# Kernel tuning notes

Measured on AMD Instinct MI355X. Metric: run time of the kernel, lower is better.

## Reference

```python
import jax, jax.numpy as jnp
import numpy as np

DIM = 1024
NUM_HEADS = 16
HEAD_DIM = DIM // NUM_HEADS
SCALING = HEAD_DIM ** (-0.5)


def setup_inputs() -> dict:
    key = jax.random.key(0)
    ks = jax.random.split(key, 9)
    B, S = 2, 2048
    s = DIM ** -0.5  # ~ torch Linear init scale
    inp = {
        "x": jax.random.normal(ks[0], (B, S, DIM), dtype=jnp.float32),
        "wq": jax.random.uniform(ks[1], (DIM, DIM), jnp.float32, -s, s),
        "bq": jax.random.uniform(ks[2], (DIM,), jnp.float32, -s, s),
        "wk": jax.random.uniform(ks[3], (DIM, DIM), jnp.float32, -s, s),
        "bk": jax.random.uniform(ks[4], (DIM,), jnp.float32, -s, s),
        "wv": jax.random.uniform(ks[5], (DIM, DIM), jnp.float32, -s, s),
        "bv": jax.random.uniform(ks[6], (DIM,), jnp.float32, -s, s),
        "wo": jax.random.uniform(ks[7], (DIM, DIM), jnp.float32, -s, s),
        "bo": jax.random.uniform(ks[8], (DIM,), jnp.float32, -s, s),
    }
    return inp


def reference(x, wq, bq, wk, bk, wv, bv, wo, bo):
    B, S, D = x.shape
    # projections (weights stored [out,in] like torch Linear -> x @ W.T + b)
    q = (x @ wq.T + bq).reshape(B, S, NUM_HEADS, HEAD_DIM)
    k = (x @ wk.T + bk).reshape(B, S, NUM_HEADS, HEAD_DIM)
    v = (x @ wv.T + bv).reshape(B, S, NUM_HEADS, HEAD_DIM)
    # [B,H,S,S] scores, scaled
    scores = jnp.einsum("bqhd,bkhd->bhqk", q, k) * SCALING
    attn = jax.nn.softmax(scores, axis=-1)
    # dropout p=0.0 (eval): identity
    out = jnp.einsum("bhqk,bkhd->bqhd", attn, v).reshape(B, S, D)
    return out @ wo.T + bo
```

## Files before the change

kernel.cpp:

```cpp
#include <hip/hip_runtime.h>

#define DIM 1024
#define NHEADS 16
#define HDIM 64
#define BATCH 2
#define SEQ 2048
#define MTOT (BATCH*SEQ)
#define QSCALE 0.18033688011112042f
#define XN ((size_t)MTOT*DIM)
#define WN ((size_t)DIM*DIM)

typedef __attribute__((ext_vector_type(8))) short short8;
typedef __attribute__((ext_vector_type(4))) float f32x4;
typedef __attribute__((ext_vector_type(16))) float f32x16;
typedef __attribute__((ext_vector_type(2))) int int2v;

static __device__ __forceinline__ unsigned short bf16rne(float f) {
    unsigned u = __builtin_bit_cast(unsigned, f);
    return (unsigned short)((u + 0x7fffu + ((u >> 16) & 1u)) >> 16);
}

static __device__ __forceinline__ void gld16(const void* g, void* l) {
    __builtin_amdgcn_global_load_lds((const __attribute__((address_space(1))) void*)g,
                                     (__attribute__((address_space(3))) void*)l, 16, 0, 0);
}

static __device__ __forceinline__ f32x16 mfma32(short8 a, short8 b, f32x16 c) {
    return __builtin_amdgcn_mfma_f32_32x32x16_bf16(a, b, c, 0, 0, 0);
}

__global__ __launch_bounds__(256)
void prep(const float* __restrict__ x, const float* __restrict__ wq, const float* __restrict__ wk,
          const float* __restrict__ wv, const float* __restrict__ wo, unsigned short* __restrict__ dst)
{
    const size_t i = ((size_t)blockIdx.x*256 + threadIdx.x)*8;
    const float* s; size_t o;
    if (i < XN)           { s = x;  o = i; }
    else if (i < XN+WN)   { s = wq; o = i - XN; }
    else if (i < XN+2*WN) { s = wk; o = i - XN - WN; }
    else if (i < XN+3*WN) { s = wv; o = i - XN - 2*WN; }
    else                  { s = wo; o = i - XN - 3*WN; }
    float4 a = *(const float4*)(s + o);
    float4 b = *(const float4*)(s + o + 4);
    uint4 w;
    w.x = (unsigned)bf16rne(a.x) | ((unsigned)bf16rne(a.y) << 16);
    w.y = (unsigned)bf16rne(a.z) | ((unsigned)bf16rne(a.w) << 16);
    w.z = (unsigned)bf16rne(b.x) | ((unsigned)bf16rne(b.y) << 16);
    w.w = (unsigned)bf16rne(b.z) | ((unsigned)bf16rne(b.w) << 16);
    *(uint4*)&dst[i] = w;
}

__global__ __launch_bounds__(256)
void gemm_qkv(const unsigned short* __restrict__ A,
              const unsigned short* __restrict__ W0, const unsigned short* __restrict__ W1,
              const unsigned short* __restrict__ W2,
              const float* __restrict__ b0, const float* __restrict__ b1, const float* __restrict__ b2,
              unsigned short* __restrict__ o0, unsigned short* __restrict__ o1, unsigned short* __restrict__ o2)
{
    __shared__ __align__(16) unsigned short As[4][4096];
    __shared__ __align__(16) unsigned short Bs[4][4096];
    const int t = threadIdx.x, wid = t >> 6, lane = t & 63;
    const int lr = lane & 15, lg = lane >> 4;
    const int bid = blockIdx.y * 24 + blockIdx.x;
    const int swz = (bid & 7) * 96 + (bid >> 3);
    const int sx = swz % 24, sy = swz / 24;
    const int widx = sx >> 3;
    const int n0 = (sx & 7) << 7;
    const int m0 = sy << 7;
    const unsigned short* W = widx == 0 ? W0 : (widx == 1 ? W1 : W2);
    const float* bias        = widx == 0 ? b0 : (widx == 1 ? b1 : b2);
    const float scale        = widx == 0 ? QSCALE : 1.0f;
    unsigned short* out      = widx == 0 ? o0 : (widx == 1 ? o1 : o2);

    const int wm = wid >> 1, wn = wid & 1;
    const int f0 = 2*wid, f1 = f0 + 1;
    const unsigned short* Ag0 = A + (size_t)(m0 + f0*16 + lr)*DIM + lg*8;
    const unsigned short* Ag1 = A + (size_t)(m0 + f1*16 + lr)*DIM + lg*8;
    const unsigned short* Bg0 = W + (size_t)(n0 + f0*16 + lr)*DIM + lg*8;
    const unsigned short* Bg1 = W + (size_t)(n0 + f1*16 + lr)*DIM + lg*8;

    auto stage = [&](int tt) {
        const int ko = (tt & 31) * 32;
        const int bb = tt & 3;
        gld16(Ag0 + ko, &As[bb][f0*512]); gld16(Ag1 + ko, &As[bb][f1*512]);
        gld16(Bg0 + ko, &Bs[bb][f0*512]); gld16(Bg1 + ko, &Bs[bb][f1*512]);
    };

    f32x4 acc[4][4] = {};
    stage(0); stage(1); stage(2);

    for (int it = 0; it < DIM/32; ++it) {
        asm volatile("s_waitcnt vmcnt(8)" ::: "memory");
        __builtin_amdgcn_s_barrier();
        const int cb = it & 3;
        short8 af[4], bf[4];
        #pragma unroll
        for (int i = 0; i < 4; ++i) af[i] = *(const short8*)&As[cb][(wm*4+i)*512 + lane*8];
        #pragma unroll
        for (int i = 0; i < 4; ++i) bf[i] = *(const short8*)&Bs[cb][(wn*4+i)*512 + lane*8];
        stage(it + 3);
        __builtin_amdgcn_s_setprio(1);
        #pragma unroll
        for (int mb = 0; mb < 4; ++mb)
            #pragma unroll
            for (int nb = 0; nb < 4; ++nb)
                acc[mb][nb] = __builtin_amdgcn_mfma_f32_16x16x32_bf16(af[mb], bf[nb], acc[mb][nb], 0, 0, 0);
        __builtin_amdgcn_s_setprio(0);
    }

    #pragma unroll
    for (int nb = 0; nb < 4; ++nb) {
        const int col = n0 + wn*64 + nb*16 + lr;
        const float bv = bias[col];
        #pragma unroll
        for (int mb = 0; mb < 4; ++mb) {
            #pragma unroll
            for (int j = 0; j < 4; ++j) {
                const int row = m0 + wm*64 + mb*16 + lg*4 + j;
                out[(size_t)row*DIM + col] = bf16rne((acc[mb][nb][j] + bv) * scale);
            }
        }
    }
}

__global__ __launch_bounds__(256)
void gemm_o(const unsigned short* __restrict__ A, const unsigned short* __restrict__ W,
            const float* __restrict__ bias, float* __restrict__ fo)
{
    __shared__ __align__(16) unsigned short As[4][2048];
    __shared__ __align__(16) unsigned short Bs[4][4096];
    const int t = threadIdx.x, wid = t >> 6, lane = t & 63;
    const int lr = lane & 15, lg = lane >> 4;
    const int bid = blockIdx.y * 8 + blockIdx.x;
    const int swz = (bid & 7) * 64 + (bid >> 3);
    const int n0 = (swz & 7) << 7;
    const int m0 = (swz >> 3) << 6;
    const int wm = wid >> 1, wn = wid & 1;

    const int fa = wid;
    const int g0 = 2*wid, g1 = g0 + 1;
    const unsigned short* Ag  = A + (size_t)(m0 + fa*16 + lr)*DIM + lg*8;
    const unsigned short* Bg0 = W + (size_t)(n0 + g0*16 + lr)*DIM + lg*8;
    const unsigned short* Bg1 = W + (size_t)(n0 + g1*16 + lr)*DIM + lg*8;

    auto stage = [&](int tt) {
        const int ko = (tt & 31) * 32;
        const int bb = tt & 3;
        gld16(Ag + ko, &As[bb][fa*512]);
        gld16(Bg0 + ko, &Bs[bb][g0*512]); gld16(Bg1 + ko, &Bs[bb][g1*512]);
    };

    f32x4 acc[2][4] = {};
    stage(0); stage(1); stage(2);

    for (int it = 0; it < DIM/32; ++it) {
        asm volatile("s_waitcnt vmcnt(6)" ::: "memory");
        __builtin_amdgcn_s_barrier();
        const int cb = it & 3;
        short8 af[2], bf[4];
        #pragma unroll
        for (int i = 0; i < 2; ++i) af[i] = *(const short8*)&As[cb][(wm*2+i)*512 + lane*8];
        #pragma unroll
        for (int i = 0; i < 4; ++i) bf[i] = *(const short8*)&Bs[cb][(wn*4+i)*512 + lane*8];
        stage(it + 3);
        __builtin_amdgcn_s_setprio(1);
        #pragma unroll
        for (int mb = 0; mb < 2; ++mb)
            #pragma unroll
            for (int nb = 0; nb < 4; ++nb)
                acc[mb][nb] = __builtin_amdgcn_mfma_f32_16x16x32_bf16(af[mb], bf[nb], acc[mb][nb], 0, 0, 0);
        __builtin_amdgcn_s_setprio(0);
    }

    #pragma unroll
    for (int nb = 0; nb < 4; ++nb) {
        const int col = n0 + wn*64 + nb*16 + lr;
        const float bv = bias[col];
        #pragma unroll
        for (int mb = 0; mb < 2; ++mb) {
            #pragma unroll
            for (int j = 0; j < 4; ++j) {
                const int row = m0 + wm*32 + mb*16 + lg*4 + j;
                fo[(size_t)row*DIM + col] = acc[mb][nb][j] + bv;
            }
        }
    }
}

__global__ __launch_bounds__(256)
void transpose_v(const unsigned short* __restrict__ V, unsigned short* __restrict__ Vt)
{
    __shared__ unsigned short tile[64][66];
    const int t  = threadIdx.x;
    const int st = blockIdx.x;
    const int bh = blockIdx.y;
    const int b = bh >> 4, h = bh & 15;
    const int sr = t >> 3;
    const int dc = (t & 7) * 8;

    #pragma unroll
    for (int r = 0; r < 2; ++r) {
        const int s = r*32 + sr;
        short8 v = *(const short8*)(V + (size_t)(b*SEQ + st*64 + s)*DIM + h*HDIM + dc);
        #pragma unroll
        for (int e = 0; e < 8; ++e) tile[s][dc + e] = (unsigned short)v[e];
    }
    __syncthreads();
    #pragma unroll
    for (int r = 0; r < 2; ++r) {
        const int d = r*32 + sr;
        short8 ov;
        #pragma unroll
        for (int e = 0; e < 8; ++e) ov[e] = (short)tile[dc + e][d];
        *(short8*)(Vt + (size_t)bh*HDIM*SEQ + (size_t)d*SEQ + st*64 + dc) = ov;
    }
}

struct PA { short8 p[4]; };

static __device__ __forceinline__ PA softmax_pack(const f32x16& s0, const f32x16& s1, float& lsum) {
    float rsum = 0.f;
    unsigned pw0[4][2], pw1[4][2];
    #pragma unroll
    for (int r1 = 0; r1 < 4; ++r1)
        #pragma unroll
        for (int tt = 0; tt < 2; ++tt) {
            float pa_ = __builtin_amdgcn_exp2f(s0[4*r1+2*tt]);
            float pb_ = __builtin_amdgcn_exp2f(s0[4*r1+2*tt+1]);
            float pc_ = __builtin_amdgcn_exp2f(s1[4*r1+2*tt]);
            float pd_ = __builtin_amdgcn_exp2f(s1[4*r1+2*tt+1]);
            rsum += (pa_ + pb_) + (pc_ + pd_);
            asm("v_cvt_pk_bf16_f32 %0, %1, %2" : "=v"(pw0[r1][tt]) : "v"(pa_), "v"(pb_));
            asm("v_cvt_pk_bf16_f32 %0, %1, %2" : "=v"(pw1[r1][tt]) : "v"(pc_), "v"(pd_));
        }
    rsum += __shfl_xor(rsum, 32);
    lsum += rsum;
    PA r;
    #pragma unroll
    for (int ss = 0; ss < 4; ++ss) {
        union { short8 s8; unsigned u[4]; } pu;
        #pragma unroll
        for (int tt = 0; tt < 2; ++tt) {
            const unsigned a = (ss >> 1) ? pw1[2*(ss&1)][tt]   : pw0[2*(ss&1)][tt];
            const unsigned b = (ss >> 1) ? pw1[2*(ss&1)+1][tt] : pw0[2*(ss&1)+1][tt];
            int2v sw = __builtin_amdgcn_permlane32_swap((int)a, (int)b, false, false);
            pu.u[tt]     = (unsigned)sw[0];
            pu.u[2 + tt] = (unsigned)sw[1];
        }
        r.p[ss] = pu.s8;
    }
    return r;
}

__global__ __launch_bounds__(256)
void attn_mfma2(const unsigned short* __restrict__ Q, const unsigned short* __restrict__ Kg,
                const unsigned short* __restrict__ Vt, unsigned short* __restrict__ O)
{
    __shared__ __align__(16) unsigned short Ks[4][4096];
    __shared__ __align__(16) unsigned short Vs[4][4096];
    const int t = threadIdx.x, wid = t >> 6, lane = t & 63;
    const int l31 = lane & 31, h = lane >> 5;
    const int bid = blockIdx.y * 16 + blockIdx.x;
    const int swz = (bid & 7) * 64 + (bid >> 3);
    const int qt = swz & 15, bh = swz >> 4;
    const int b = bh >> 4, hh = bh & 15;
    const size_t qkbase = (size_t)b*SEQ*DIM + (size_t)hh*HDIM;
    const unsigned short* Qb = Q + qkbase;
    const unsigned short* Kb = Kg + qkbase;
    const unsigned short* Vb = Vt + (size_t)bh*HDIM*SEQ;
    unsigned short*       Ob = O + qkbase;
    const int q0 = qt*128 + wid*32;

    short8 qf[4];
    #pragma unroll
    for (int ds = 0; ds < 4; ++ds)
        qf[ds] = *(const short8*)&Qb[(size_t)(q0 + l31)*DIM + ds*16 + h*8];

    const int f0 = 2*wid, f1 = f0 + 1;
    const unsigned short* Kg0 = &Kb[(size_t)((f0>>2)*32 + l31)*DIM + (f0&3)*16 + h*8];
    const unsigned short* Kg1 = &Kb[(size_t)((f1>>2)*32 + l31)*DIM + (f1&3)*16 + h*8];
    const unsigned short* Vg0 = &Vb[(size_t)((f0>>2)*32 + l31)*SEQ + (f0&3)*16 + h*8];
    const unsigned short* Vg1 = &Vb[(size_t)((f1>>2)*32 + l31)*SEQ + (f1&3)*16 + h*8];

    auto stage = [&](int tn) {
        const size_t koK = (size_t)tn * 64 * DIM;
        const size_t koV = (size_t)tn * 64;
        const int bb = tn & 3;
        gld16(Kg0 + koK, &Ks[bb][f0*512]); gld16(Kg1 + koK, &Ks[bb][f1*512]);
        gld16(Vg0 + koV, &Vs[bb][f0*512]); gld16(Vg1 + koV, &Vs[bb][f1*512]);
    };

    f32x16 ctx0 = {}, ctx1 = {};
    float lsum = 0.0f;

    stage(0); stage(1);

    for (int w = 0; w < SEQ/128; ++w) {
        const int t0 = 2*w;
        const int ba = t0 & 3, bb2 = (t0+1) & 3;
        __syncthreads();
        if (w + 1 < SEQ/128) { stage(t0+2); stage(t0+3); }

        f32x16 s0a = {}, s1a = {};
        __builtin_amdgcn_s_setprio(1);
        #pragma unroll
        for (int ds = 0; ds < 4; ++ds) {
            short8 kf0 = *(const short8*)&Ks[ba][ds*512 + lane*8];
            short8 kf1 = *(const short8*)&Ks[ba][(4+ds)*512 + lane*8];
            s0a = mfma32(kf0, qf[ds], s0a);
            s1a = mfma32(kf1, qf[ds], s1a);
        }
        __builtin_amdgcn_s_setprio(0);

        PA pa = softmax_pack(s0a, s1a, lsum);

        f32x16 s0b = {}, s1b = {};
        __builtin_amdgcn_s_setprio(1);
        #pragma unroll
        for (int ds = 0; ds < 4; ++ds) {
            short8 kf0 = *(const short8*)&Ks[bb2][ds*512 + lane*8];
            short8 kf1 = *(const short8*)&Ks[bb2][(4+ds)*512 + lane*8];
            s0b = mfma32(kf0, qf[ds], s0b);
            s1b = mfma32(kf1, qf[ds], s1b);
        }
        #pragma unroll
        for (int ss = 0; ss < 4; ++ss) {
            short8 vf0 = *(const short8*)&Vs[ba][ss*512 + lane*8];
            short8 vf1 = *(const short8*)&Vs[ba][(4+ss)*512 + lane*8];
            ctx0 = mfma32(pa.p[ss], vf0, ctx0);
            ctx1 = mfma32(pa.p[ss], vf1, ctx1);
        }
        __builtin_amdgcn_s_setprio(0);

        PA pb = softmax_pack(s0b, s1b, lsum);

        __builtin_amdgcn_s_setprio(1);
        #pragma unroll
        for (int ss = 0; ss < 4; ++ss) {
            short8 vf0 = *(const short8*)&Vs[bb2][ss*512 + lane*8];
            short8 vf1 = *(const short8*)&Vs[bb2][(4+ss)*512 + lane*8];
            ctx0 = mfma32(pb.p[ss], vf0, ctx0);
            ctx1 = mfma32(pb.p[ss], vf1, ctx1);
        }
        __builtin_amdgcn_s_setprio(0);
    }

    const float linv = 1.0f / lsum;
    #pragma unroll
    for (int r = 0; r < 16; ++r) {
        const int qrow = (r&3) + 8*(r>>2) + 4*h;
        const float nm = __shfl(linv, qrow);
        unsigned short* p = &Ob[(size_t)(q0 + qrow)*DIM + l31];
        p[0]  = bf16rne(ctx0[r] * nm);
        p[32] = bf16rne(ctx1[r] * nm);
    }
}

extern "C" void kernel_launch(void* const* d_in, const int* in_sizes, int n_in,
                              void* d_out, int out_size, void* d_ws, size_t ws_size,
                              hipStream_t stream) {
    const float* x  = (const float*)d_in[0];
    const float* wq = (const float*)d_in[1];
    const float* bq = (const float*)d_in[2];
    const float* wk = (const float*)d_in[3];
    const float* bk = (const float*)d_in[4];
    const float* wv = (const float*)d_in[5];
    const float* bv = (const float*)d_in[6];
    const float* wo = (const float*)d_in[7];
    const float* bo = (const float*)d_in[8];
    float* out = (float*)d_out;

    unsigned short* Xb  = (unsigned short*)d_ws;
    unsigned short* Wqb = Xb  + XN;
    unsigned short* Wkb = Wqb + WN;
    unsigned short* Wvb = Wkb + WN;
    unsigned short* Wob = Wvb + WN;
    unsigned short* Qb  = Wob + WN;
    unsigned short* Kb  = Qb  + XN;
    unsigned short* Vb  = Kb  + XN;
    unsigned short* Vtb = Vb  + XN;
    unsigned short* Cb  = Xb;

    prep<<<4096, 256, 0, stream>>>(x, wq, wk, wv, wo, Xb);

    gemm_qkv<<<dim3(24, 32), 256, 0, stream>>>(Xb, Wqb, Wkb, Wvb, bq, bk, bv, Qb, Kb, Vb);

    transpose_v<<<dim3(SEQ/64, BATCH*NHEADS), 256, 0, stream>>>(Vb, Vtb);
    attn_mfma2<<<dim3(SEQ/128, BATCH*NHEADS), 256, 0, stream>>>(Qb, Kb, Vtb, Cb);

    gemm_o<<<dim3(8, 64), 256, 0, stream>>>(Cb, Wob, bo, out);
}
```

Measured before the change: 151.9 us.

## Shrink GEMM LDS ring to three stages and split attention prefetch waits

The QKV and output-projection GEMMs go from a 4-slot, 3-ahead LDS ring to a 3-slot, 2-ahead ring with rotating slot indices, adjusted vmcnt waits and an explicit drain on the last iterations. This cuts LDS use per block, which may let more blocks fit per CU, at the cost of a shallower prefetch distance. In the attention kernel, the single __syncthreads plus two-tile prefetch per iteration becomes two finer vmcnt-wait-and-barrier points, each issuing one tile's prefetch. The aim is to start waiting on loads later and overlap them better with the softmax and MFMA work.

```diff
diff --git a/kernel.cpp b/kernel.cpp
--- a/kernel.cpp
+++ b/kernel.cpp
@@ -57,8 +57,8 @@
               const float* __restrict__ b0, const float* __restrict__ b1, const float* __restrict__ b2,
               unsigned short* __restrict__ o0, unsigned short* __restrict__ o1, unsigned short* __restrict__ o2)
 {
-    __shared__ __align__(16) unsigned short As[4][4096];
-    __shared__ __align__(16) unsigned short Bs[4][4096];
+    __shared__ __align__(16) unsigned short As[3][4096];
+    __shared__ __align__(16) unsigned short Bs[3][4096];
     const int t = threadIdx.x, wid = t >> 6, lane = t & 63;
     const int lr = lane & 15, lg = lane >> 4;
     const int bid = blockIdx.y * 24 + blockIdx.x;
@@ -79,26 +79,26 @@
     const unsigned short* Bg0 = W + (size_t)(n0 + f0*16 + lr)*DIM + lg*8;
     const unsigned short* Bg1 = W + (size_t)(n0 + f1*16 + lr)*DIM + lg*8;
 
-    auto stage = [&](int tt) {
-        const int ko = (tt & 31) * 32;
-        const int bb = tt & 3;
-        gld16(Ag0 + ko, &As[bb][f0*512]); gld16(Ag1 + ko, &As[bb][f1*512]);
-        gld16(Bg0 + ko, &Bs[bb][f0*512]); gld16(Bg1 + ko, &Bs[bb][f1*512]);
+    auto stage = [&](int tt, int slot) {
+        const int ko = tt * 32;
+        gld16(Ag0 + ko, &As[slot][f0*512]); gld16(Ag1 + ko, &As[slot][f1*512]);
+        gld16(Bg0 + ko, &Bs[slot][f0*512]); gld16(Bg1 + ko, &Bs[slot][f1*512]);
     };
 
     f32x4 acc[4][4] = {};
-    stage(0); stage(1); stage(2);
+    stage(0, 0); stage(1, 1);
+    int c0 = 0, c1 = 1, c2 = 2;
 
     for (int it = 0; it < DIM/32; ++it) {
-        asm volatile("s_waitcnt vmcnt(8)" ::: "memory");
+        if (it < DIM/32 - 2) { asm volatile("s_waitcnt vmcnt(4)" ::: "memory"); }
+        else                 { asm volatile("s_waitcnt vmcnt(0)" ::: "memory"); }
         __builtin_amdgcn_s_barrier();
-        const int cb = it & 3;
         short8 af[4], bf[4];
         #pragma unroll
-        for (int i = 0; i < 4; ++i) af[i] = *(const short8*)&As[cb][(wm*4+i)*512 + lane*8];
-        #pragma unroll
-        for (int i = 0; i < 4; ++i) bf[i] = *(const short8*)&Bs[cb][(wn*4+i)*512 + lane*8];
-        stage(it + 3);
+        for (int i = 0; i < 4; ++i) af[i] = *(const short8*)&As[c0][(wm*4+i)*512 + lane*8];
+        #pragma unroll
+        for (int i = 0; i < 4; ++i) bf[i] = *(const short8*)&Bs[c0][(wn*4+i)*512 + lane*8];
+        if (it + 2 < DIM/32) stage(it + 2, c2);
         __builtin_amdgcn_s_setprio(1);
         #pragma unroll
         for (int mb = 0; mb < 4; ++mb)
@@ -106,6 +106,7 @@
             for (int nb = 0; nb < 4; ++nb)
                 acc[mb][nb] = __builtin_amdgcn_mfma_f32_16x16x32_bf16(af[mb], bf[nb], acc[mb][nb], 0, 0, 0);
         __builtin_amdgcn_s_setprio(0);
+        const int tmp = c0; c0 = c1; c1 = c2; c2 = tmp;
     }
 
     #pragma unroll
@@ -127,8 +128,8 @@
 void gemm_o(const unsigned short* __restrict__ A, const unsigned short* __restrict__ W,
             const float* __restrict__ bias, float* __restrict__ fo)
 {
-    __shared__ __align__(16) unsigned short As[4][2048];
-    __shared__ __align__(16) unsigned short Bs[4][4096];
+    __shared__ __align__(16) unsigned short As[3][2048];
+    __shared__ __align__(16) unsigned short Bs[3][4096];
     const int t = threadIdx.x, wid = t >> 6, lane = t & 63;
     const int lr = lane & 15, lg = lane >> 4;
     const int bid = blockIdx.y * 8 + blockIdx.x;
@@ -143,26 +144,26 @@
     const unsigned short* Bg0 = W + (size_t)(n0 + g0*16 + lr)*DIM + lg*8;
     const unsigned short* Bg1 = W + (size_t)(n0 + g1*16 + lr)*DIM + lg*8;
 
-    auto stage = [&](int tt) {
-        const int ko = (tt & 31) * 32;
-        const int bb = tt & 3;
-        gld16(Ag + ko, &As[bb][fa*512]);
-        gld16(Bg0 + ko, &Bs[bb][g0*512]); gld16(Bg1 + ko, &Bs[bb][g1*512]);
+    auto stage = [&](int tt, int slot) {
+        const int ko = tt * 32;
+        gld16(Ag + ko, &As[slot][fa*512]);
+        gld16(Bg0 + ko, &Bs[slot][g0*512]); gld16(Bg1 + ko, &Bs[slot][g1*512]);
     };
 
     f32x4 acc[2][4] = {};
-    stage(0); stage(1); stage(2);
+    stage(0, 0); stage(1, 1);
+    int c0 = 0, c1 = 1, c2 = 2;
 
     for (int it = 0; it < DIM/32; ++it) {
-        asm volatile("s_waitcnt vmcnt(6)" ::: "memory");
+        if (it < DIM/32 - 2) { asm volatile("s_waitcnt vmcnt(3)" ::: "memory"); }
+        else                 { asm volatile("s_waitcnt vmcnt(0)" ::: "memory"); }
         __builtin_amdgcn_s_barrier();
-        const int cb = it & 3;
         short8 af[2], bf[4];
         #pragma unroll
-        for (int i = 0; i < 2; ++i) af[i] = *(const short8*)&As[cb][(wm*2+i)*512 + lane*8];
-        #pragma unroll
-        for (int i = 0; i < 4; ++i) bf[i] = *(const short8*)&Bs[cb][(wn*4+i)*512 + lane*8];
-        stage(it + 3);
+        for (int i = 0; i < 2; ++i) af[i] = *(const short8*)&As[c0][(wm*2+i)*512 + lane*8];
+        #pragma unroll
+        for (int i = 0; i < 4; ++i) bf[i] = *(const short8*)&Bs[c0][(wn*4+i)*512 + lane*8];
+        if (it + 2 < DIM/32) stage(it + 2, c2);
         __builtin_amdgcn_s_setprio(1);
         #pragma unroll
         for (int mb = 0; mb < 2; ++mb)
@@ -170,6 +171,7 @@
             for (int nb = 0; nb < 4; ++nb)
                 acc[mb][nb] = __builtin_amdgcn_mfma_f32_16x16x32_bf16(af[mb], bf[nb], acc[mb][nb], 0, 0, 0);
         __builtin_amdgcn_s_setprio(0);
+        const int tmp = c0; c0 = c1; c1 = c2; c2 = tmp;
     }
 
     #pragma unroll
@@ -295,11 +297,16 @@
 
     stage(0); stage(1);
 
-    for (int w = 0; w < SEQ/128; ++w) {
+    const int NW = SEQ/128;
+    for (int w = 0; w < NW; ++w) {
         const int t0 = 2*w;
         const int ba = t0 & 3, bb2 = (t0+1) & 3;
-        __syncthreads();
-        if (w + 1 < SEQ/128) { stage(t0+2); stage(t0+3); }
+        const bool more = (w + 1 < NW);
+
+        if (more) { asm volatile("s_waitcnt vmcnt(4)" ::: "memory"); }
+        else      { asm volatile("s_waitcnt vmcnt(0)" ::: "memory"); }
+        __builtin_amdgcn_s_barrier();
+        if (more) stage(t0 + 2);
 
         f32x16 s0a = {}, s1a = {};
         __builtin_amdgcn_s_setprio(1);
@@ -313,6 +320,11 @@
         __builtin_amdgcn_s_setprio(0);
 
         PA pa = softmax_pack(s0a, s1a, lsum);
+
+        if (more) { asm volatile("s_waitcnt vmcnt(4)" ::: "memory"); }
+        else      { asm volatile("s_waitcnt vmcnt(0)" ::: "memory"); }
+        __builtin_amdgcn_s_barrier();
+        if (more) stage(t0 + 3);
 
         f32x16 s0b = {}, s1b = {};
         __builtin_amdgcn_s_setprio(1);
```

After: 141.9 us. 1.07x faster.
